# Kernel optimization log

Measured on AMD Instinct MI355X. Metric: run time of the kernel, lower is better.

## Reference

```python
import jax, jax.numpy as jnp
import numpy as np

N = 600_000            # active input voxels
CIN, COUT = 64, 128    # IN_CHANNELS, NUM_BEV_FEATURES
B, Z, Y, X = 4, 16, 468, 468  # sparse grid (Waymo-like); conv halves Z
BN_EPS = 1e-5


def setup_inputs() -> dict:
    rng = np.random.default_rng(0)
    # unique active voxel coordinates
    lin = rng.choice(B * Z * Y * X, size=N, replace=False)
    b = lin // (Z * Y * X)
    r = lin % (Z * Y * X)
    z = r // (Y * X)
    r = r % (Y * X)
    y = r // X
    x = r % X
    # spconv rulebook for kernel (2,1,1), stride (2,1,1), pad 0:
    # tap id along z and output segment id from unique (b, z//2, y, x)
    kz = (z % 2).astype(np.int32)
    keys = ((b * (Z // 2) + z // 2) * Y + y) * X + x
    _, inv = np.unique(keys, return_inverse=True)
    out_ids = inv.astype(np.int32)
    n_out = np.int32(out_ids.max() + 1)

    key = jax.random.key(0)
    ks = jax.random.split(key, 6)
    return {
        "features": jax.random.normal(ks[0], (N, CIN), dtype=jnp.float32),
        "W": jax.random.normal(ks[1], (2, CIN, COUT), dtype=jnp.float32) * 0.05,
        "gamma": jax.random.uniform(ks[2], (COUT,), dtype=jnp.float32, minval=0.5, maxval=1.5),
        "beta": jax.random.normal(ks[3], (COUT,), dtype=jnp.float32) * 0.1,
        "running_mean": jax.random.normal(ks[4], (COUT,), dtype=jnp.float32) * 0.1,
        "running_var": jax.random.uniform(ks[5], (COUT,), dtype=jnp.float32, minval=0.5, maxval=1.5),
        "kz": jnp.asarray(kz),
        "out_ids": jnp.asarray(out_ids),
        "n_out": jnp.asarray(n_out),
    }


def reference(features, W, gamma, beta, running_mean, running_var, kz, out_ids, n_out):
    # gather-GEMM: one GEMM per kernel tap, select by tap id
    y0 = features @ W[0]                       # [N, COUT]
    y1 = features @ W[1]
    contrib = jnp.where((kz == 0)[:, None], y0, y1)
    # scatter-add into output voxels (padded to N segments for static shape)
    out = jax.ops.segment_sum(contrib, out_ids, num_segments=N)  # [N, COUT]
    # BatchNorm1d (eval) + ReLU, fused into scatter output pass
    inv_std = gamma * jax.lax.rsqrt(running_var + BN_EPS)
    out = jax.nn.relu((out - running_mean) * inv_std + beta)
    # zero out padding rows beyond the true number of output voxels
    valid = (jnp.arange(N) < n_out)[:, None]
    return jnp.where(valid, out, 0.0)
```

## Files before the change

kernel.cpp:

```cpp
#include <hip/hip_runtime.h>
#include <stdint.h>

#define CIN 64
#define COUT 128
#define BLOCK 256
#define WT_STRIDE 136

typedef __attribute__((ext_vector_type(8))) __bf16 bf16x8;
typedef __attribute__((ext_vector_type(8))) unsigned short ushort8;
typedef __attribute__((ext_vector_type(4))) float f32x4;

__device__ __forceinline__ unsigned short f2bf(float f) {
    uint32_t u = __float_as_uint(f);
    u = (u + 0x7FFFu + ((u >> 16) & 1u)) >> 16;
    return (unsigned short)u;
}

__global__ void scatter_inv_kernel(const int* __restrict__ kz,
                                   const int* __restrict__ oid,
                                   int* __restrict__ inv0,
                                   int* __restrict__ inv1,
                                   int n) {
    int i = blockIdx.x * blockDim.x + threadIdx.x;
    if (i < n) {
        int o = oid[i];
        if (kz[i] == 0) inv0[o] = i + 1;
        else            inv1[o] = i + 1;
    }
}

__launch_bounds__(BLOCK, 4)
__global__ void spconv_bn_relu_kernel(const float* __restrict__ feat,
                                      const float* __restrict__ W,
                                      const float* __restrict__ gamma,
                                      const float* __restrict__ beta,
                                      const float* __restrict__ rmean,
                                      const float* __restrict__ rvar,
                                      const int* __restrict__ inv0,
                                      const int* __restrict__ inv1,
                                      const int* __restrict__ n_out_p,
                                      float* __restrict__ out,
                                      int N, int num_wtiles) {
    __shared__ unsigned short lds_wT[COUT * WT_STRIDE];
    __shared__ __align__(16) float lds_scale[COUT];
    __shared__ __align__(16) float lds_bias[COUT];

    const int tid = threadIdx.x;
    const int nout = *n_out_p;

    const float4* W4 = (const float4*)W;
    #pragma unroll
    for (int u = 0; u < 16; ++u) {
        int flat4 = u * BLOCK + tid;
        int n4 = flat4 & 31;
        int k  = flat4 >> 5;
        float4 v = W4[flat4];
        int nb = n4 * 4;
        lds_wT[(nb + 0) * WT_STRIDE + k] = f2bf(v.x);
        lds_wT[(nb + 1) * WT_STRIDE + k] = f2bf(v.y);
        lds_wT[(nb + 2) * WT_STRIDE + k] = f2bf(v.z);
        lds_wT[(nb + 3) * WT_STRIDE + k] = f2bf(v.w);
    }
    if (tid < COUT) {
        float s = gamma[tid] * rsqrtf(rvar[tid] + 1e-5f);
        lds_scale[tid] = s;
        lds_bias[tid]  = fmaf(-rmean[tid], s, beta[tid]);
    }
    __syncthreads();

    const float4* feat4 = (const float4*)feat;
    const int wave = tid >> 6;
    const int lane = tid & 63;
    const int lrow = lane & 15;
    const int quad = lane >> 4;

    const int gwave   = blockIdx.x * (BLOCK / 64) + wave;
    const int wstride = gridDim.x * (BLOCK / 64);

    int i0 = 0, i1 = 0;
    if (gwave < num_wtiles) {
        int row = gwave * 16 + lrow;
        if (row < N) { i0 = inv0[row]; i1 = inv1[row]; }
    }

    for (int wt = gwave; wt < num_wtiles; wt += wstride) {
        const int row = wt * 16 + lrow;

        float4 ra[4], rb[4];
        #pragma unroll
        for (int s = 0; s < 4; ++s) {
            int idx = (s < 2) ? i0 : i1;
            ra[s] = make_float4(0.f, 0.f, 0.f, 0.f);
            rb[s] = make_float4(0.f, 0.f, 0.f, 0.f);
            if (idx > 0) {
                const float4* p = feat4 + (size_t)(idx - 1) * 16 + (s & 1) * 8 + quad * 2;
                ra[s] = p[0];
                rb[s] = p[1];
            }
        }

        int nwt = wt + wstride;
        int p0 = 0, p1 = 0;
        if (nwt < num_wtiles) {
            int nr = nwt * 16 + lrow;
            if (nr < N) { p0 = inv0[nr]; p1 = inv1[nr]; }
        }

        bf16x8 afrag[4];
        #pragma unroll
        for (int s = 0; s < 4; ++s) {
            ushort8 u;
            u[0] = f2bf(ra[s].x); u[1] = f2bf(ra[s].y);
            u[2] = f2bf(ra[s].z); u[3] = f2bf(ra[s].w);
            u[4] = f2bf(rb[s].x); u[5] = f2bf(rb[s].y);
            u[6] = f2bf(rb[s].z); u[7] = f2bf(rb[s].w);
            afrag[s] = __builtin_bit_cast(bf16x8, u);
        }

        #pragma unroll
        for (int c = 0; c < 8; ++c) {
            const unsigned short* bbase = &lds_wT[(c * 16 + lrow) * WT_STRIDE + quad * 8];
            f32x4 acc = {0.f, 0.f, 0.f, 0.f};
            #pragma unroll
            for (int s = 0; s < 4; ++s) {
                bf16x8 wfrag = __builtin_bit_cast(bf16x8, *(const ushort8*)(bbase + s * 32));
                acc = __builtin_amdgcn_mfma_f32_16x16x32_bf16(wfrag, afrag[s], acc, 0, 0, 0);
            }
            if (row < N) {
                const int col = c * 16 + quad * 4;
                float4 o4 = make_float4(0.f, 0.f, 0.f, 0.f);
                if (row < nout) {
                    f32x4 sc = *(const f32x4*)&lds_scale[col];
                    f32x4 bi = *(const f32x4*)&lds_bias[col];
                    o4.x = fmaxf(fmaf(acc[0], sc[0], bi[0]), 0.f);
                    o4.y = fmaxf(fmaf(acc[1], sc[1], bi[1]), 0.f);
                    o4.z = fmaxf(fmaf(acc[2], sc[2], bi[2]), 0.f);
                    o4.w = fmaxf(fmaf(acc[3], sc[3], bi[3]), 0.f);
                }
                *(float4*)&out[(size_t)row * COUT + col] = o4;
            }
        }

        i0 = p0; i1 = p1;
    }
}

extern "C" void kernel_launch(void* const* d_in, const int* in_sizes, int n_in,
                              void* d_out, int out_size, void* d_ws, size_t ws_size,
                              hipStream_t stream) {
    const float* feat  = (const float*)d_in[0];
    const float* W     = (const float*)d_in[1];
    const float* gamma = (const float*)d_in[2];
    const float* beta  = (const float*)d_in[3];
    const float* rmean = (const float*)d_in[4];
    const float* rvar  = (const float*)d_in[5];
    const int*   kz    = (const int*)d_in[6];
    const int*   oid   = (const int*)d_in[7];
    const int*   noutp = (const int*)d_in[8];
    float* out = (float*)d_out;

    const int N = in_sizes[6];

    int* inv0 = (int*)d_ws;
    int* inv1 = inv0 + N;

    hipMemsetAsync(d_ws, 0, (size_t)2 * N * sizeof(int), stream);

    int sb = (N + 255) / 256;
    scatter_inv_kernel<<<sb, 256, 0, stream>>>(kz, oid, inv0, inv1, N);

    int num_wtiles = (N + 15) / 16;
    int nblocks = (num_wtiles + 3) / 4;
    int grid = nblocks < 1024 ? nblocks : 1024;
    spconv_bn_relu_kernel<<<grid, BLOCK, 0, stream>>>(
        feat, W, gamma, beta, rmean, rvar, inv0, inv1, noutp, out, N, num_wtiles);
}
```

Baseline: 567.3 us.

## Prefetch next tile's gathered features and restage via LDS for coalesced loads

The feature gather is reorganized so that each group of 8 lanes reads one full 256-byte input row, making global loads contiguous. The data is converted to bf16 and staged in per-wave LDS, and the MFMA A-fragments are read back from there. The gather for the next tile is issued before the current tile's MFMAs, a software-pipelining step meant to hide gather latency. The cost is extra LDS space and more registers, so occupancy is lowered to 3 blocks per SIMD and the grid is capped at 768.

```diff
diff --git a/kernel.cpp b/kernel.cpp
--- a/kernel.cpp
+++ b/kernel.cpp
@@ -4,7 +4,9 @@
 #define CIN 64
 #define COUT 128
 #define BLOCK 256
+#define WPB 4
 #define WT_STRIDE 136
+#define SEG_STRIDE 144
 
 typedef __attribute__((ext_vector_type(8))) __bf16 bf16x8;
 typedef __attribute__((ext_vector_type(8))) unsigned short ushort8;
@@ -29,7 +31,7 @@
     }
 }
 
-__launch_bounds__(BLOCK, 4)
+__launch_bounds__(BLOCK, 3)
 __global__ void spconv_bn_relu_kernel(const float* __restrict__ feat,
                                       const float* __restrict__ W,
                                       const float* __restrict__ gamma,
@@ -42,6 +44,7 @@
                                       float* __restrict__ out,
                                       int N, int num_wtiles) {
     __shared__ unsigned short lds_wT[COUT * WT_STRIDE];
+    __shared__ __align__(16) unsigned char lds_stage[WPB * 32 * SEG_STRIDE];
     __shared__ __align__(16) float lds_scale[COUT];
     __shared__ __align__(16) float lds_bias[COUT];
 
@@ -69,13 +72,17 @@
     __syncthreads();
 
     const float4* feat4 = (const float4*)feat;
-    const int wave = tid >> 6;
-    const int lane = tid & 63;
-    const int lrow = lane & 15;
-    const int quad = lane >> 4;
-
-    const int gwave   = blockIdx.x * (BLOCK / 64) + wave;
-    const int wstride = gridDim.x * (BLOCK / 64);
+    const int wave   = tid >> 6;
+    const int lane   = tid & 63;
+    const int lrow   = lane & 15;
+    const int quad   = lane >> 4;
+    const int lseg   = lane >> 3;
+    const int lchunk = lane & 7;
+
+    unsigned char* stg = lds_stage + wave * (32 * SEG_STRIDE);
+
+    const int gwave   = blockIdx.x * WPB + wave;
+    const int wstride = gridDim.x * WPB;
 
     int i0 = 0, i1 = 0;
     if (gwave < num_wtiles) {
@@ -83,21 +90,23 @@
         if (row < N) { i0 = inv0[row]; i1 = inv1[row]; }
     }
 
+    float4 ga[4], gb[4];
+    #pragma unroll
+    for (int r = 0; r < 4; ++r) {
+        int seg = r * 8 + lseg;
+        int rs  = seg & 15;
+        int idx = (seg & 16) ? __shfl(i1, rs, 64) : __shfl(i0, rs, 64);
+        ga[r] = make_float4(0.f, 0.f, 0.f, 0.f);
+        gb[r] = ga[r];
+        if (idx > 0) {
+            const float4* p = feat4 + (size_t)(idx - 1) * 16 + lchunk * 2;
+            ga[r] = p[0];
+            gb[r] = p[1];
+        }
+    }
+
     for (int wt = gwave; wt < num_wtiles; wt += wstride) {
         const int row = wt * 16 + lrow;
-
-        float4 ra[4], rb[4];
-        #pragma unroll
-        for (int s = 0; s < 4; ++s) {
-            int idx = (s < 2) ? i0 : i1;
-            ra[s] = make_float4(0.f, 0.f, 0.f, 0.f);
-            rb[s] = make_float4(0.f, 0.f, 0.f, 0.f);
-            if (idx > 0) {
-                const float4* p = feat4 + (size_t)(idx - 1) * 16 + (s & 1) * 8 + quad * 2;
-                ra[s] = p[0];
-                rb[s] = p[1];
-            }
-        }
 
         int nwt = wt + wstride;
         int p0 = 0, p1 = 0;
@@ -106,15 +115,38 @@
             if (nr < N) { p0 = inv0[nr]; p1 = inv1[nr]; }
         }
 
+        #pragma unroll
+        for (int r = 0; r < 4; ++r) {
+            int seg = r * 8 + lseg;
+            ushort8 u;
+            u[0] = f2bf(ga[r].x); u[1] = f2bf(ga[r].y);
+            u[2] = f2bf(ga[r].z); u[3] = f2bf(ga[r].w);
+            u[4] = f2bf(gb[r].x); u[5] = f2bf(gb[r].y);
+            u[6] = f2bf(gb[r].z); u[7] = f2bf(gb[r].w);
+            *(ushort8*)(stg + seg * SEG_STRIDE + lchunk * 16) = u;
+        }
+
+        float4 na[4], nb[4];
+        #pragma unroll
+        for (int r = 0; r < 4; ++r) {
+            int seg = r * 8 + lseg;
+            int rs  = seg & 15;
+            int idx = (seg & 16) ? __shfl(p1, rs, 64) : __shfl(p0, rs, 64);
+            na[r] = make_float4(0.f, 0.f, 0.f, 0.f);
+            nb[r] = na[r];
+            if (idx > 0) {
+                const float4* p = feat4 + (size_t)(idx - 1) * 16 + lchunk * 2;
+                na[r] = p[0];
+                nb[r] = p[1];
+            }
+        }
+
         bf16x8 afrag[4];
         #pragma unroll
         for (int s = 0; s < 4; ++s) {
-            ushort8 u;
-            u[0] = f2bf(ra[s].x); u[1] = f2bf(ra[s].y);
-            u[2] = f2bf(ra[s].z); u[3] = f2bf(ra[s].w);
-            u[4] = f2bf(rb[s].x); u[5] = f2bf(rb[s].y);
-            u[6] = f2bf(rb[s].z); u[7] = f2bf(rb[s].w);
-            afrag[s] = __builtin_bit_cast(bf16x8, u);
+            int seg = (s >> 1) * 16 + lrow;
+            afrag[s] = __builtin_bit_cast(bf16x8,
+                *(const ushort8*)(stg + seg * SEG_STRIDE + (s & 1) * 64 + quad * 16));
         }
 
         #pragma unroll
@@ -142,6 +174,8 @@
         }
 
         i0 = p0; i1 = p1;
+        #pragma unroll
+        for (int r = 0; r < 4; ++r) { ga[r] = na[r]; gb[r] = nb[r]; }
     }
 }
 
@@ -170,8 +204,8 @@
     scatter_inv_kernel<<<sb, 256, 0, stream>>>(kz, oid, inv0, inv1, N);
 
     int num_wtiles = (N + 15) / 16;
-    int nblocks = (num_wtiles + 3) / 4;
-    int grid = nblocks < 1024 ? nblocks : 1024;
+    int nblocks = (num_wtiles + WPB - 1) / WPB;
+    int grid = nblocks < 768 ? nblocks : 768;
     spconv_bn_relu_kernel<<<grid, BLOCK, 0, stream>>>(
         feat, W, gamma, beta, rmean, rvar, inv0, inv1, noutp, out, N, num_wtiles);
 }
```

Measured after the change: 562.7 us. About the same (-0.8%).

## Double-buffer feature gathers with coalesced row loads staged through LDS

Applied to the files above, without the earlier changes.

Restructures the main loop so two tiles' feature gathers are in flight at once: the gather for the tile two steps ahead is issued before the current tile is computed, and inverse indices are prefetched four steps ahead. Each group of 8 lanes now reads one full 256-byte feature row, so loads are contiguous. The rows are converted to bf16 and staged in a per-wave LDS buffer from which MFMA fragments are read. Output stores become nontemporal and launch bounds drop to 3 blocks per CU, trading occupancy and extra LDS and registers for more memory-level parallelism in the latency-bound gather.

```diff
diff --git a/kernel.cpp b/kernel.cpp
--- a/kernel.cpp
+++ b/kernel.cpp
@@ -4,7 +4,9 @@
 #define CIN 64
 #define COUT 128
 #define BLOCK 256
+#define WPB 4
 #define WT_STRIDE 136
+#define SEG_STRIDE 144
 
 typedef __attribute__((ext_vector_type(8))) __bf16 bf16x8;
 typedef __attribute__((ext_vector_type(8))) unsigned short ushort8;
@@ -29,7 +31,7 @@
     }
 }
 
-__launch_bounds__(BLOCK, 4)
+__launch_bounds__(BLOCK, 3)
 __global__ void spconv_bn_relu_kernel(const float* __restrict__ feat,
                                       const float* __restrict__ W,
                                       const float* __restrict__ gamma,
@@ -42,6 +44,7 @@
                                       float* __restrict__ out,
                                       int N, int num_wtiles) {
     __shared__ unsigned short lds_wT[COUT * WT_STRIDE];
+    __shared__ __align__(16) unsigned char lds_stage[WPB * 32 * SEG_STRIDE];
     __shared__ __align__(16) float lds_scale[COUT];
     __shared__ __align__(16) float lds_bias[COUT];
 
@@ -69,80 +72,121 @@
     __syncthreads();
 
     const float4* feat4 = (const float4*)feat;
-    const int wave = tid >> 6;
-    const int lane = tid & 63;
-    const int lrow = lane & 15;
-    const int quad = lane >> 4;
-
-    const int gwave   = blockIdx.x * (BLOCK / 64) + wave;
-    const int wstride = gridDim.x * (BLOCK / 64);
-
-    int i0 = 0, i1 = 0;
-    if (gwave < num_wtiles) {
-        int row = gwave * 16 + lrow;
-        if (row < N) { i0 = inv0[row]; i1 = inv1[row]; }
-    }
-
-    for (int wt = gwave; wt < num_wtiles; wt += wstride) {
-        const int row = wt * 16 + lrow;
-
-        float4 ra[4], rb[4];
-        #pragma unroll
-        for (int s = 0; s < 4; ++s) {
-            int idx = (s < 2) ? i0 : i1;
-            ra[s] = make_float4(0.f, 0.f, 0.f, 0.f);
-            rb[s] = make_float4(0.f, 0.f, 0.f, 0.f);
-            if (idx > 0) {
-                const float4* p = feat4 + (size_t)(idx - 1) * 16 + (s & 1) * 8 + quad * 2;
-                ra[s] = p[0];
-                rb[s] = p[1];
-            }
+    const int wave   = tid >> 6;
+    const int lane   = tid & 63;
+    const int lrow   = lane & 15;
+    const int quad   = lane >> 4;
+    const int lseg   = lane >> 3;
+    const int lchunk = lane & 7;
+
+    unsigned char* stg = lds_stage + wave * (32 * SEG_STRIDE);
+
+    const int gwave   = blockIdx.x * WPB + wave;
+    const int wstride = gridDim.x * WPB;
+
+#define LOAD_INV(WT, J0, J1) do {                                         \
+        (J0) = 0; (J1) = 0;                                               \
+        if ((WT) < num_wtiles) {                                          \
+            int _r = (WT) * 16 + lrow;                                    \
+            if (_r < N) { (J0) = inv0[_r]; (J1) = inv1[_r]; }             \
+        }                                                                 \
+    } while (0)
+
+#define ISSUE_GATHER(J0, J1, GA, GB) do {                                 \
+        _Pragma("unroll")                                                 \
+        for (int _r = 0; _r < 4; ++_r) {                                  \
+            int _seg = _r * 8 + lseg;                                     \
+            int _rs  = _seg & 15;                                         \
+            int _idx = (_seg & 16) ? __shfl((J1), _rs, 64)                \
+                                   : __shfl((J0), _rs, 64);               \
+            GA[_r] = make_float4(0.f, 0.f, 0.f, 0.f);                     \
+            GB[_r] = GA[_r];                                              \
+            if (_idx > 0) {                                               \
+                const float4* _p = feat4 + (size_t)(_idx - 1) * 16 + lchunk * 2; \
+                GA[_r] = _p[0];                                           \
+                GB[_r] = _p[1];                                           \
+            }                                                             \
+        }                                                                 \
+    } while (0)
+
+#define STAGE(GA, GB) do {                                                \
+        _Pragma("unroll")                                                 \
+        for (int _r = 0; _r < 4; ++_r) {                                  \
+            int _seg = _r * 8 + lseg;                                     \
+            ushort8 _u;                                                   \
+            _u[0] = f2bf(GA[_r].x); _u[1] = f2bf(GA[_r].y);               \
+            _u[2] = f2bf(GA[_r].z); _u[3] = f2bf(GA[_r].w);               \
+            _u[4] = f2bf(GB[_r].x); _u[5] = f2bf(GB[_r].y);               \
+            _u[6] = f2bf(GB[_r].z); _u[7] = f2bf(GB[_r].w);               \
+            *(ushort8*)(stg + _seg * SEG_STRIDE + lchunk * 16) = _u;      \
+        }                                                                 \
+    } while (0)
+
+#define COMPUTE_STORE(WT) do {                                            \
+        const int _row = (WT) * 16 + lrow;                                \
+        bf16x8 _af[4];                                                    \
+        _Pragma("unroll")                                                 \
+        for (int _s = 0; _s < 4; ++_s) {                                  \
+            int _sg = (_s >> 1) * 16 + lrow;                              \
+            _af[_s] = __builtin_bit_cast(bf16x8,                          \
+                *(const ushort8*)(stg + _sg * SEG_STRIDE + (_s & 1) * 64 + quad * 16)); \
+        }                                                                 \
+        _Pragma("unroll")                                                 \
+        for (int _c = 0; _c < 8; ++_c) {                                  \
+            const unsigned short* _bb = &lds_wT[(_c * 16 + lrow) * WT_STRIDE + quad * 8]; \
+            f32x4 _acc = {0.f, 0.f, 0.f, 0.f};                            \
+            _Pragma("unroll")                                             \
+            for (int _s = 0; _s < 4; ++_s) {                              \
+                bf16x8 _wf = __builtin_bit_cast(bf16x8, *(const ushort8*)(_bb + _s * 32)); \
+                _acc = __builtin_amdgcn_mfma_f32_16x16x32_bf16(_wf, _af[_s], _acc, 0, 0, 0); \
+            }                                                             \
+            if (_row < N) {                                               \
+                const int _col = _c * 16 + quad * 4;                      \
+                f32x4 _o4 = {0.f, 0.f, 0.f, 0.f};                         \
+                if (_row < nout) {                                        \
+                    f32x4 _sc = *(const f32x4*)&lds_scale[_col];          \
+                    f32x4 _bi = *(const f32x4*)&lds_bias[_col];           \
+                    _o4[0] = fmaxf(fmaf(_acc[0], _sc[0], _bi[0]), 0.f);   \
+                    _o4[1] = fmaxf(fmaf(_acc[1], _sc[1], _bi[1]), 0.f);   \
+                    _o4[2] = fmaxf(fmaf(_acc[2], _sc[2], _bi[2]), 0.f);   \
+                    _o4[3] = fmaxf(fmaf(_acc[3], _sc[3], _bi[3]), 0.f);   \
+                }                                                         \
+                __builtin_nontemporal_store(_o4,                          \
+                    (f32x4*)&out[(size_t)_row * COUT + _col]);            \
+            }                                                             \
+        }                                                                 \
+    } while (0)
+
+    int wt = gwave;
+    int jA0, jA1, jB0, jB1, pA0, pA1, pB0, pB1;
+    float4 gaA[4], gbA[4], gaB[4], gbB[4];
+
+    LOAD_INV(wt, jA0, jA1);
+    ISSUE_GATHER(jA0, jA1, gaA, gbA);
+    LOAD_INV(wt + wstride, jB0, jB1);
+    ISSUE_GATHER(jB0, jB1, gaB, gbB);
+    LOAD_INV(wt + 2 * wstride, pA0, pA1);
+    LOAD_INV(wt + 3 * wstride, pB0, pB1);
+
+    for (; wt < num_wtiles; wt += 2 * wstride) {
+        STAGE(gaA, gbA);
+        ISSUE_GATHER(pA0, pA1, gaA, gbA);
+        LOAD_INV(wt + 4 * wstride, pA0, pA1);
+        COMPUTE_STORE(wt);
+
+        int wtB = wt + wstride;
+        if (wtB < num_wtiles) {
+            STAGE(gaB, gbB);
+            ISSUE_GATHER(pB0, pB1, gaB, gbB);
+            LOAD_INV(wtB + 4 * wstride, pB0, pB1);
+            COMPUTE_STORE(wtB);
         }
-
-        int nwt = wt + wstride;
-        int p0 = 0, p1 = 0;
-        if (nwt < num_wtiles) {
-            int nr = nwt * 16 + lrow;
-            if (nr < N) { p0 = inv0[nr]; p1 = inv1[nr]; }
-        }
-
-        bf16x8 afrag[4];
-        #pragma unroll
-        for (int s = 0; s < 4; ++s) {
-            ushort8 u;
-            u[0] = f2bf(ra[s].x); u[1] = f2bf(ra[s].y);
-            u[2] = f2bf(ra[s].z); u[3] = f2bf(ra[s].w);
-            u[4] = f2bf(rb[s].x); u[5] = f2bf(rb[s].y);
-            u[6] = f2bf(rb[s].z); u[7] = f2bf(rb[s].w);
-            afrag[s] = __builtin_bit_cast(bf16x8, u);
-        }
-
-        #pragma unroll
-        for (int c = 0; c < 8; ++c) {
-            const unsigned short* bbase = &lds_wT[(c * 16 + lrow) * WT_STRIDE + quad * 8];
-            f32x4 acc = {0.f, 0.f, 0.f, 0.f};
-            #pragma unroll
-            for (int s = 0; s < 4; ++s) {
-                bf16x8 wfrag = __builtin_bit_cast(bf16x8, *(const ushort8*)(bbase + s * 32));
-                acc = __builtin_amdgcn_mfma_f32_16x16x32_bf16(wfrag, afrag[s], acc, 0, 0, 0);
-            }
-            if (row < N) {
-                const int col = c * 16 + quad * 4;
-                float4 o4 = make_float4(0.f, 0.f, 0.f, 0.f);
-                if (row < nout) {
-                    f32x4 sc = *(const f32x4*)&lds_scale[col];
-                    f32x4 bi = *(const f32x4*)&lds_bias[col];
-                    o4.x = fmaxf(fmaf(acc[0], sc[0], bi[0]), 0.f);
-                    o4.y = fmaxf(fmaf(acc[1], sc[1], bi[1]), 0.f);
-                    o4.z = fmaxf(fmaf(acc[2], sc[2], bi[2]), 0.f);
-                    o4.w = fmaxf(fmaf(acc[3], sc[3], bi[3]), 0.f);
-                }
-                *(float4*)&out[(size_t)row * COUT + col] = o4;
-            }
-        }
-
-        i0 = p0; i1 = p1;
-    }
+    }
+
+#undef LOAD_INV
+#undef ISSUE_GATHER
+#undef STAGE
+#undef COMPUTE_STORE
 }
 
 extern "C" void kernel_launch(void* const* d_in, const int* in_sizes, int n_in,
@@ -164,13 +208,13 @@
     int* inv0 = (int*)d_ws;
     int* inv1 = inv0 + N;
 
-    hipMemsetAsync(d_ws, 0, (size_t)2 * N * sizeof(int), stream);
+    (void)hipMemsetAsync(d_ws, 0, (size_t)2 * N * sizeof(int), stream);
 
     int sb = (N + 255) / 256;
     scatter_inv_kernel<<<sb, 256, 0, stream>>>(kz, oid, inv0, inv1, N);
 
     int num_wtiles = (N + 15) / 16;
-    int nblocks = (num_wtiles + 3) / 4;
+    int nblocks = (num_wtiles + WPB - 1) / WPB;
     int grid = nblocks < 1024 ? nblocks : 1024;
     spconv_bn_relu_kernel<<<grid, BLOCK, 0, stream>>>(
         feat, W, gamma, beta, rmean, rvar, inv0, inv1, noutp, out, N, num_wtiles);
```

After: 589.0 us. +3.8%, slower.
